# Performance work log

Measured on AMD Instinct MI355X. Metric: run time of the kernel, lower is better.

Reference implementation:

```python
import jax, jax.numpy as jnp
import numpy as np

T, B, H = 2048, 16, 1024


def setup_inputs() -> dict:
    key = jax.random.key(0)
    k1, k2, k3 = jax.random.split(key, 3)
    inputs = jax.random.normal(k1, (T, B, H), dtype=jnp.float32)
    # torch params initialized uniform_(-0.1, 0.1)
    weight_W = jax.random.uniform(k2, (H, H), dtype=jnp.float32, minval=-0.1, maxval=0.1)
    weight_proj = jax.random.uniform(k3, (H, 1), dtype=jnp.float32, minval=-0.1, maxval=0.1)
    return {"inputs": inputs, "weight_W": weight_W, "weight_proj": weight_proj,
            "attention_width": 3}


def reference(inputs, weight_W, weight_proj, attention_width):
    # inputs: [T, B, H] (time-major). For t < w the input passes through unchanged.
    # For t >= w: attend over the previous w steps (t-w .. t-1, excluding t):
    #   score_j = tanh(h_j @ W) @ proj, a = softmax over window, out = sum_j a_j * h_j
    w = attention_width
    t = inputs.shape[0]
    n = t - w  # number of attended output positions
    # per-position scores, computed once for all timesteps: [T, B]
    scores = jnp.squeeze(jnp.tanh(inputs @ weight_W) @ weight_proj, axis=-1)
    # sliding windows via w shifted views (w is small and static)
    s_win = jnp.stack([scores[j:j + n] for j in range(w)], axis=0)   # [w, n, B]
    v_win = jnp.stack([inputs[j:j + n] for j in range(w)], axis=0)   # [w, n, B, H]
    attn = jax.nn.softmax(s_win, axis=0)                             # softmax over window
    tail = jnp.einsum('wnb,wnbh->nbh', attn, v_win)                  # [n, B, H]
    return jnp.concatenate([inputs[:w], tail], axis=0)               # [T, B, H]
```

## Files before the change

### kernel.cpp

```cpp
#include <hip/hip_runtime.h>
#include <stdint.h>

#define T_DIM 2048
#define B_DIM 16
#define H_DIM 1024
#define M_DIM (T_DIM * B_DIM)
#define BK 64

typedef __attribute__((ext_vector_type(8))) short bf16x8;
typedef __attribute__((ext_vector_type(4))) float floatx4;

__device__ inline unsigned short f2bf(float f) {
  union { float f; unsigned int u; } c; c.f = f;
  unsigned int u = c.u;
  return (unsigned short)((u + 0x7FFFu + ((u >> 16) & 1u)) >> 16);
}

__device__ inline float fast_tanh(float x) {
  float e = __expf(2.0f * x);
  return 1.0f - 2.0f / (e + 1.0f);
}

__global__ void convert_x_kernel(const float* __restrict__ x,
                                 unsigned short* __restrict__ xb) {
  size_t i = ((size_t)blockIdx.x * 256 + threadIdx.x) * 4;
  float4 v = *(const float4*)(x + i);
  ushort4 o;
  o.x = f2bf(v.x); o.y = f2bf(v.y); o.z = f2bf(v.z); o.w = f2bf(v.w);
  *(ushort4*)(xb + i) = o;
}

__global__ void transpose_w_kernel(const float* __restrict__ w,
                                   unsigned short* __restrict__ wt) {
  __shared__ float tile[32][33];
  int tx = threadIdx.x, ty = threadIdx.y;
  int n0 = blockIdx.x * 32, k0 = blockIdx.y * 32;
  for (int i = ty; i < 32; i += 8)
    tile[i][tx] = w[(size_t)(k0 + i) * H_DIM + n0 + tx];
  __syncthreads();
  for (int i = ty; i < 32; i += 8)
    wt[(size_t)(n0 + i) * H_DIM + k0 + tx] = f2bf(tile[tx][i]);
}

__global__ __launch_bounds__(256, 3)
void score_gemm_kernel(const unsigned short* __restrict__ Xb,
                       const unsigned short* __restrict__ Wt,
                       const float* __restrict__ proj,
                       float* __restrict__ scores) {
  __shared__ __align__(16) unsigned short ldsA[128 * BK];
  __shared__ __align__(16) unsigned short ldsB[128 * BK];

  const int tid  = threadIdx.x;
  const int lane = tid & 63;
  const int wave = tid >> 6;
  const int wy = wave >> 1, wx = wave & 1;
  const int quad = lane >> 4, l16 = lane & 15;

  const int bm    = blockIdx.x >> 2;
  const int split = blockIdx.x & 3;
  const int m0 = bm * 128;
  const int nbase = split * 256;

  int ldsOff[4];
  int rowOff[4];
  #pragma unroll
  for (int i = 0; i < 4; ++i) {
    int cb = (i * 4 + wave) * 64;
    int s = cb + lane;
    int row = s >> 3, cs = s & 7;
    int cg = cs ^ (row & 7);
    ldsOff[i] = cb;
    rowOff[i] = row * H_DIM + cg * 8;
  }

  float sc[4][4];
  #pragma unroll
  for (int a = 0; a < 4; ++a)
    #pragma unroll
    for (int b = 0; b < 4; ++b) sc[a][b] = 0.0f;

  for (int n0 = nbase; n0 < nbase + 256; n0 += 128) {
    floatx4 acc[4][4];
    #pragma unroll
    for (int a = 0; a < 4; ++a)
      #pragma unroll
      for (int b = 0; b < 4; ++b) acc[a][b] = (floatx4){0.f, 0.f, 0.f, 0.f};

    for (int k0 = 0; k0 < H_DIM; k0 += BK) {
      #pragma unroll
      for (int i = 0; i < 4; ++i) {
        const unsigned short* ga = Xb + (size_t)m0 * H_DIM + rowOff[i] + k0;
        __builtin_amdgcn_global_load_lds(
            (const __attribute__((address_space(1))) void*)ga,
            (__attribute__((address_space(3))) void*)(&ldsA[ldsOff[i] * 8]),
            16, 0, 0);
        const unsigned short* gb = Wt + (size_t)n0 * H_DIM + rowOff[i] + k0;
        __builtin_amdgcn_global_load_lds(
            (const __attribute__((address_space(1))) void*)gb,
            (__attribute__((address_space(3))) void*)(&ldsB[ldsOff[i] * 8]),
            16, 0, 0);
      }
      __syncthreads();

      #pragma unroll
      for (int kk = 0; kk < BK; kk += 32) {
        const int c = (kk >> 3) + quad;
        bf16x8 af[4], bfr[4];
        #pragma unroll
        for (int rs = 0; rs < 4; ++rs) {
          int r = wy * 64 + rs * 16 + l16;
          af[rs] = *(const bf16x8*)&ldsA[(r * 8 + (c ^ (r & 7))) * 8];
        }
        #pragma unroll
        for (int ns = 0; ns < 4; ++ns) {
          int n = wx * 64 + ns * 16 + l16;
          bfr[ns] = *(const bf16x8*)&ldsB[(n * 8 + (c ^ (n & 7))) * 8];
        }
        #pragma unroll
        for (int rs = 0; rs < 4; ++rs)
          #pragma unroll
          for (int ns = 0; ns < 4; ++ns)
            acc[rs][ns] = __builtin_amdgcn_mfma_f32_16x16x32_bf16(
                af[rs], bfr[ns], acc[rs][ns], 0, 0, 0);
      }
      __syncthreads();
    }

    #pragma unroll
    for (int ns = 0; ns < 4; ++ns) {
      int n = n0 + wx * 64 + ns * 16 + l16;
      float p = proj[n];
      #pragma unroll
      for (int rs = 0; rs < 4; ++rs)
        #pragma unroll
        for (int g = 0; g < 4; ++g)
          sc[rs][g] += fast_tanh(acc[rs][ns][g]) * p;
    }
  }

  #pragma unroll
  for (int rs = 0; rs < 4; ++rs)
    #pragma unroll
    for (int g = 0; g < 4; ++g) {
      float v = sc[rs][g];
      v += __shfl_xor(v, 1);
      v += __shfl_xor(v, 2);
      v += __shfl_xor(v, 4);
      v += __shfl_xor(v, 8);
      if (l16 == 0) {
        int row = m0 + wy * 64 + rs * 16 + quad * 4 + g;
        atomicAdd(&scores[row], v);
      }
    }
}

__global__ void out_kernel(const float* __restrict__ x,
                           const float* __restrict__ scores,
                           const int* __restrict__ wp,
                           float* __restrict__ out) {
  int r = blockIdx.x;
  int t = r >> 4, b = r & 15;
  int w = *wp;
  if (w > 8) w = 8;
  int h = threadIdx.x;
  const float4* x4 = (const float4*)x;
  float4* o4 = (float4*)out;
  size_t base = (size_t)r * 256 + h;
  if (t < w) { o4[base] = x4[base]; return; }
  float s[8];
  float mx = -1e30f;
  for (int j = 0; j < w; ++j) {
    s[j] = scores[(t - w + j) * B_DIM + b];
    mx = fmaxf(mx, s[j]);
  }
  float sum = 0.f;
  for (int j = 0; j < w; ++j) { s[j] = __expf(s[j] - mx); sum += s[j]; }
  float inv = 1.0f / sum;
  float4 o = {0.f, 0.f, 0.f, 0.f};
  for (int j = 0; j < w; ++j) {
    float a = s[j] * inv;
    float4 v = x4[((size_t)(t - w + j) * B_DIM + b) * 256 + h];
    o.x += a * v.x; o.y += a * v.y; o.z += a * v.z; o.w += a * v.w;
  }
  o4[base] = o;
}

extern "C" void kernel_launch(void* const* d_in, const int* in_sizes, int n_in,
                              void* d_out, int out_size, void* d_ws, size_t ws_size,
                              hipStream_t stream) {
  const float* x    = (const float*)d_in[0];
  const float* w    = (const float*)d_in[1];
  const float* proj = (const float*)d_in[2];
  const int*   wp   = (const int*)d_in[3];
  float* out = (float*)d_out;

  unsigned short* Xb = (unsigned short*)d_out;
  unsigned short* Wt = (unsigned short*)((char*)d_out + (size_t)64 * 1024 * 1024);
  float* scores = (float*)d_ws;

  hipMemsetAsync(scores, 0, M_DIM * sizeof(float), stream);

  convert_x_kernel<<<M_DIM * H_DIM / 1024, 256, 0, stream>>>(x, Xb);
  transpose_w_kernel<<<dim3(32, 32), dim3(32, 8), 0, stream>>>(w, Wt);
  score_gemm_kernel<<<1024, 256, 0, stream>>>(Xb, Wt, proj, scores);
  out_kernel<<<M_DIM, 256, 0, stream>>>(x, scores, wp, out);
}
```

Before: 370.2 us.

## Reuse sliding-window rows in out kernel and group GEMM blocks for L2 reuse

```diff
diff --git a/kernel.cpp b/kernel.cpp
--- a/kernel.cpp
+++ b/kernel.cpp
@@ -6,6 +6,7 @@
 #define H_DIM 1024
 #define M_DIM (T_DIM * B_DIM)
 #define BK 64
+#define TCHUNK 8
 
 typedef __attribute__((ext_vector_type(8))) short bf16x8;
 typedef __attribute__((ext_vector_type(4))) float floatx4;
@@ -42,7 +43,7 @@
     wt[(size_t)(n0 + i) * H_DIM + k0 + tx] = f2bf(tile[tx][i]);
 }
 
-__global__ __launch_bounds__(256, 3)
+__global__ __launch_bounds__(256, 4)
 void score_gemm_kernel(const unsigned short* __restrict__ Xb,
                        const unsigned short* __restrict__ Wt,
                        const float* __restrict__ proj,
@@ -56,9 +57,12 @@
   const int wy = wave >> 1, wx = wave & 1;
   const int quad = lane >> 4, l16 = lane & 15;
 
-  const int bm    = blockIdx.x >> 2;
-  const int split = blockIdx.x & 3;
-  const int m0 = bm * 128;
+  const int idx   = blockIdx.x;
+  const int x7    = idx & 7;
+  const int split = (idx >> 3) & 3;
+  const int g     = idx >> 5;
+  const int bm    = g * 8 + x7;
+  const int m0    = bm * 128;
   const int nbase = split * 256;
 
   int ldsOff[4];
@@ -133,22 +137,22 @@
       #pragma unroll
       for (int rs = 0; rs < 4; ++rs)
         #pragma unroll
-        for (int g = 0; g < 4; ++g)
-          sc[rs][g] += fast_tanh(acc[rs][ns][g]) * p;
+        for (int gg = 0; gg < 4; ++gg)
+          sc[rs][gg] += fast_tanh(acc[rs][ns][gg]) * p;
     }
   }
 
   #pragma unroll
   for (int rs = 0; rs < 4; ++rs)
     #pragma unroll
-    for (int g = 0; g < 4; ++g) {
-      float v = sc[rs][g];
+    for (int gg = 0; gg < 4; ++gg) {
+      float v = sc[rs][gg];
       v += __shfl_xor(v, 1);
       v += __shfl_xor(v, 2);
       v += __shfl_xor(v, 4);
       v += __shfl_xor(v, 8);
       if (l16 == 0) {
-        int row = m0 + wy * 64 + rs * 16 + quad * 4 + g;
+        int row = m0 + wy * 64 + rs * 16 + quad * 4 + gg;
         atomicAdd(&scores[row], v);
       }
     }
@@ -158,31 +162,75 @@
                            const float* __restrict__ scores,
                            const int* __restrict__ wp,
                            float* __restrict__ out) {
-  int r = blockIdx.x;
-  int t = r >> 4, b = r & 15;
   int w = *wp;
-  if (w > 8) w = 8;
-  int h = threadIdx.x;
+  int t0 = blockIdx.x * TCHUNK;
+  int b  = blockIdx.y;
+  int h  = threadIdx.x;
   const float4* x4 = (const float4*)x;
   float4* o4 = (float4*)out;
-  size_t base = (size_t)r * 256 + h;
-  if (t < w) { o4[base] = x4[base]; return; }
-  float s[8];
-  float mx = -1e30f;
-  for (int j = 0; j < w; ++j) {
-    s[j] = scores[(t - w + j) * B_DIM + b];
-    mx = fmaxf(mx, s[j]);
+
+  if (w == 3) {
+    float4 z = {0.f, 0.f, 0.f, 0.f};
+    float4 a0, a1, a2;
+    float  s0, s1, s2;
+    {
+      int tm = t0 - 3;
+      a0 = (tm >= 0) ? x4[((size_t)tm * B_DIM + b) * 256 + h] : z;
+      s0 = (tm >= 0) ? scores[tm * B_DIM + b] : 0.f;
+      tm = t0 - 2;
+      a1 = (tm >= 0) ? x4[((size_t)tm * B_DIM + b) * 256 + h] : z;
+      s1 = (tm >= 0) ? scores[tm * B_DIM + b] : 0.f;
+      tm = t0 - 1;
+      a2 = (tm >= 0) ? x4[((size_t)tm * B_DIM + b) * 256 + h] : z;
+      s2 = (tm >= 0) ? scores[tm * B_DIM + b] : 0.f;
+    }
+    #pragma unroll
+    for (int i = 0; i < TCHUNK; ++i) {
+      int t = t0 + i;
+      size_t rbase = ((size_t)t * B_DIM + b) * 256 + h;
+      float4 v = x4[rbase];
+      float  sv = scores[t * B_DIM + b];
+      if (t < 3) {
+        o4[rbase] = v;
+      } else {
+        float m = fmaxf(fmaxf(s0, s1), s2);
+        float e0 = __expf(s0 - m), e1 = __expf(s1 - m), e2 = __expf(s2 - m);
+        float inv = 1.0f / (e0 + e1 + e2);
+        e0 *= inv; e1 *= inv; e2 *= inv;
+        float4 o;
+        o.x = e0 * a0.x + e1 * a1.x + e2 * a2.x;
+        o.y = e0 * a0.y + e1 * a1.y + e2 * a2.y;
+        o.z = e0 * a0.z + e1 * a1.z + e2 * a2.z;
+        o.w = e0 * a0.w + e1 * a1.w + e2 * a2.w;
+        o4[rbase] = o;
+      }
+      a0 = a1; a1 = a2; a2 = v;
+      s0 = s1; s1 = s2; s2 = sv;
+    }
+  } else {
+    if (w > 8) w = 8;
+    for (int i = 0; i < TCHUNK; ++i) {
+      int t = t0 + i;
+      size_t rbase = ((size_t)t * B_DIM + b) * 256 + h;
+      if (t < w) { o4[rbase] = x4[rbase]; continue; }
+      float s[8];
+      float mx = -1e30f;
+      for (int j = 0; j < w; ++j) {
+        s[j] = scores[(t - w + j) * B_DIM + b];
+        mx = fmaxf(mx, s[j]);
+      }
+      float sum = 0.f;
+      for (int j = 0; j < w; ++j) { s[j] = __expf(s[j] - mx); sum += s[j]; }
+      float inv = 1.0f / sum;
+      float4 o = {0.f, 0.f, 0.f, 0.f};
+      for (int j = 0; j < w; ++j) {
+        float a = s[j] * inv;
+        float4 v = x4[((size_t)(t - w + j) * B_DIM + b) * 256 + h];
+        o.x += a * v.x; o.y += a * v.y; o.z += a * v.z; o.w += a * v.w;
+      }
+      o4[rbase] = o;
+    }
   }
-  float sum = 0.f;
-  for (int j = 0; j < w; ++j) { s[j] = __expf(s[j] - mx); sum += s[j]; }
-  float inv = 1.0f / sum;
-  float4 o = {0.f, 0.f, 0.f, 0.f};
-  for (int j = 0; j < w; ++j) {
-    float a = s[j] * inv;
-    float4 v = x4[((size_t)(t - w + j) * B_DIM + b) * 256 + h];
-    o.x += a * v.x; o.y += a * v.y; o.z += a * v.z; o.w += a * v.w;
-  }
-  o4[base] = o;
 }
 
 extern "C" void kernel_launch(void* const* d_in, const int* in_sizes, int n_in,
@@ -203,5 +251,5 @@
   convert_x_kernel<<<M_DIM * H_DIM / 1024, 256, 0, stream>>>(x, Xb);
   transpose_w_kernel<<<dim3(32, 32), dim3(32, 8), 0, stream>>>(w, Wt);
   score_gemm_kernel<<<1024, 256, 0, stream>>>(Xb, Wt, proj, scores);
-  out_kernel<<<M_DIM, 256, 0, stream>>>(x, scores, wp, out);
-}
+  out_kernel<<<dim3(T_DIM / TCHUNK, B_DIM), 256, 0, stream>>>(x, scores, wp, out);
+}
```

After: 353.2 us. 4.6% less time.
